# Kernel optimization log

Measured on AMD Instinct MI355X. Metric: run time of the kernel, lower is better.

Reference implementation:

```python
import jax, jax.numpy as jnp
import numpy as np

D = 1024
H = 4
HD = D // H
WIN = 128
NPMEM = 4
EPS = 1e-5


def _layernorm(x, g, b):
    mu = jnp.mean(x, axis=-1, keepdims=True)
    var = jnp.var(x, axis=-1, keepdims=True)
    return (x - mu) * jax.lax.rsqrt(var + EPS) * g + b


def _rotate_half(t):
    h = t.shape[-1] // 2
    return jnp.concatenate([-t[..., h:], t[..., :h]], axis=-1)


def setup_inputs() -> dict:
    key = jax.random.key(0)
    ks = jax.random.split(key, 20)
    B, L = 2, 4096
    s = 0.02
    inp = {
        'x': jax.random.normal(ks[0], (B, L, D), jnp.float32),
        'cos': jax.random.uniform(ks[1], (L + 8, HD), jnp.float32),
        'sin': jax.random.uniform(ks[2], (L + 8, HD), jnp.float32),
        'global_out': jax.random.normal(ks[3], (B, L, D), jnp.float32),
        'local_out': jax.random.normal(ks[4], (B, L, D), jnp.float32),
        'wq': jax.random.normal(ks[5], (D, D), jnp.float32) * s,
        'wk': jax.random.normal(ks[6], (D, D), jnp.float32) * s,
        'wv': jax.random.normal(ks[7], (D, D), jnp.float32) * s,
        'wo_attn': jax.random.normal(ks[8], (D, D), jnp.float32) * s,
        'pmem': jax.random.normal(ks[9], (1, NPMEM, D), jnp.float32),
        'gate_w': jax.random.normal(ks[10], (3 * D, 3 * D), jnp.float32) * s,
        'gate_b': jnp.zeros((3 * D,), jnp.float32),
        'outproj_w': jax.random.normal(ks[11], (3 * D, D), jnp.float32) * s,
        'outproj_b': jnp.zeros((D,), jnp.float32),
        'ln_mem_g': jnp.ones((D,), jnp.float32),
        'ln_mem_b': jnp.zeros((D,), jnp.float32),
        'ln_mlp_g': jnp.ones((D,), jnp.float32),
        'ln_mlp_b': jnp.zeros((D,), jnp.float32),
        'fc1_w': jax.random.normal(ks[12], (D, 4 * D), jnp.float32) * s,
        'fc1_b': jnp.zeros((4 * D,), jnp.float32),
        'fc2_w': jax.random.normal(ks[13], (4 * D, D), jnp.float32) * s,
        'fc2_b': jnp.zeros((D,), jnp.float32),
    }
    return inp


def reference(x, cos, sin, global_out, local_out, wq, wk, wv, wo_attn, pmem,
              gate_w, gate_b, outproj_w, outproj_b, ln_mem_g, ln_mem_b,
              ln_mlp_g, ln_mlp_b, fc1_w, fc1_b, fc2_w, fc2_b):
    B, L, _ = x.shape
    residual = x

    # prepend persistent memory tokens
    xp = jnp.concatenate([jnp.broadcast_to(pmem, (B, NPMEM, D)), x], axis=1)
    Lt = L + NPMEM

    q = (xp @ wq).reshape(B, Lt, H, HD)
    k = (xp @ wk).reshape(B, Lt, H, HD)
    v = (xp @ wv).reshape(B, Lt, H, HD)

    # rotary embedding over the full pmem+seq length
    cc = cos[:Lt][None, :, None, :]
    ss = sin[:Lt][None, :, None, :]
    q = q * cc + _rotate_half(q) * ss
    k = k * cc + _rotate_half(k) * ss

    i = jnp.arange(Lt)[:, None]
    j = jnp.arange(Lt)[None, :]
    mask = (j <= i) & (j >= i - WIN)  # [Lt, Lt]

    scale = 1.0 / jnp.sqrt(jnp.asarray(HD, x.dtype))
    scores = jnp.einsum('blhd,bmhd->bhlm', q, k) * scale
    scores = jnp.where(mask[None, None], scores, jnp.finfo(scores.dtype).min)
    attn = jax.nn.softmax(scores, axis=-1)
    out = jnp.einsum('bhlm,bmhd->blhd', attn, v).reshape(B, Lt, D)
    core_out = (out @ wo_attn)[:, -L:, :]

    combined = jnp.concatenate([global_out, local_out, core_out], axis=-1)
    g = jax.nn.sigmoid(combined @ gate_w + gate_b)
    memory_output = (combined * g) @ outproj_w + outproj_b

    x1 = residual + _layernorm(memory_output, ln_mem_g, ln_mem_b)
    xn = _layernorm(x1, ln_mlp_g, ln_mlp_b)
    mlp_out = jax.nn.silu(xn @ fc1_w + fc1_b) @ fc2_w + fc2_b
    return x1 + mlp_out
```

## Files before the change

kernel.cpp:

```cpp
#include <hip/hip_runtime.h>
#include <stdint.h>

#define D_    1024
#define H_    4
#define HD_   256
#define WIN_  128
#define NPM_  4
#define B_    2
#define L_    4096
#define LT_   4100
#define LTP_  4112
#define QKL_  2048

typedef __attribute__((ext_vector_type(8))) short short8;
typedef __attribute__((ext_vector_type(4))) float f32x4;

__device__ __forceinline__ short f2bf(float f) {
  union { float f; uint32_t u; } v; v.f = f;
  uint32_t r = v.u + 0x7FFFu + ((v.u >> 16) & 1u);
  return (short)(r >> 16);
}
__device__ __forceinline__ float bf2f(short h) {
  union { uint32_t u; float f; } v; v.u = ((uint32_t)(uint16_t)h) << 16;
  return v.f;
}

typedef __attribute__((address_space(1))) void GAS;
typedef __attribute__((address_space(3))) void LAS;
__device__ __forceinline__ void gl16(const void* g, void* l) {
  __builtin_amdgcn_global_load_lds((GAS*)g, (LAS*)l, 16, 0, 0);
}
__device__ __forceinline__ void waitvm0() { asm volatile("s_waitcnt vmcnt(0)" ::: "memory"); }

#define EP_BF16 0
#define EP_F32B 1
#define EP_GATE 2
#define EP_SILU 3
#define EP_RES  4
#define EP_CORE 5
#define EP_VT   6

template<int EP, int TM>
__global__ __launch_bounds__(256, 4)
void gemm_bt(const short* __restrict__ A, int lda,
             const short* __restrict__ Bt,
             void* __restrict__ Cp, int ldc,
             const float* __restrict__ bias,
             const void* __restrict__ aux, int ldaux,
             int M, int N, int K)
{
  constexpr int WM = TM / 2;
  constexpr int MT = WM / 16;
  constexpr int BUFSZ = (TM + 128) * 32;
  __shared__ __attribute__((aligned(16))) short lds[2 * BUFSZ];
  const int tid  = threadIdx.x;
  const int lane = tid & 63, wave = tid >> 6;
  const int lhi  = lane >> 4, llo = lane & 15;
  const int m0 = blockIdx.x * TM, n0 = blockIdx.y * 128;
  const int mw = (wave >> 1) * WM, nw = (wave & 1) * 64;

  const int srow = tid >> 2;
  const int sg   = (tid & 3) ^ ((tid >> 3) & 3);
  const short* pA0 = A + (size_t)min(m0 + srow, M - 1) * lda + sg * 8;
  const short* pA1 = (TM == 128) ? A + (size_t)min(m0 + srow + 64, M - 1) * lda + sg * 8 : pA0;
  const short* pB0 = Bt + (size_t)(n0 + srow) * K + sg * 8;
  const short* pB1 = Bt + (size_t)(n0 + srow + 64) * K + sg * 8;

  const int segoff = (lhi ^ ((llo >> 1) & 3)) * 8;

  auto stage = [&](int b, int i) {
    const int k = i << 5;
    short* base = &lds[b * BUFSZ];
    gl16(pA0 + k, &base[tid * 8]);
    if constexpr (TM == 128) gl16(pA1 + k, &base[2048 + tid * 8]);
    gl16(pB0 + k, &base[TM * 32 + tid * 8]);
    gl16(pB1 + k, &base[TM * 32 + 2048 + tid * 8]);
  };

  f32x4 acc[MT][4];
#pragma unroll
  for (int i = 0; i < MT; i++)
#pragma unroll
    for (int j = 0; j < 4; j++) acc[i][j] = f32x4{0.f, 0.f, 0.f, 0.f};

  const int NI = K >> 5;
  stage(0, 0);
  waitvm0();
  __syncthreads();

  for (int i = 0; i < NI; i++) {
    if (i + 1 < NI) stage((i + 1) & 1, i + 1);
    const short* bufp = &lds[(i & 1) * BUFSZ];
    short8 af[MT], bfr[4];
#pragma unroll
    for (int mt = 0; mt < MT; mt++)
      af[mt] = *(const short8*)&bufp[(mw + mt * 16 + llo) * 32 + segoff];
#pragma unroll
    for (int nt = 0; nt < 4; nt++)
      bfr[nt] = *(const short8*)&bufp[TM * 32 + (nw + nt * 16 + llo) * 32 + segoff];
#pragma unroll
    for (int mt = 0; mt < MT; mt++)
#pragma unroll
      for (int nt = 0; nt < 4; nt++)
        acc[mt][nt] = __builtin_amdgcn_mfma_f32_16x16x32_bf16(af[mt], bfr[nt], acc[mt][nt], 0, 0, 0);
    waitvm0();
    __syncthreads();
  }

  const int gcb = n0 + nw;
#pragma unroll
  for (int mt = 0; mt < MT; mt++) {
    const int gr0 = m0 + mw + mt * 16 + lhi * 4;
#pragma unroll
    for (int nt = 0; nt < 4; nt++) {
      const int gc = gcb + nt * 16 + llo;
      float bv = 0.f;
      if constexpr (EP != EP_BF16 && EP != EP_CORE && EP != EP_VT) bv = bias[gc];
#pragma unroll
      for (int r = 0; r < 4; r++) {
        const int gr = gr0 + r;
        if (gr >= M) continue;
        const float v = acc[mt][nt][r];
        if constexpr (EP == EP_VT) {
          if (gc < N) {
            const int b   = gc >= LT_ ? 1 : 0;
            const int tok = gc - b * LT_;
            const int hh  = gr >> 8, dd = gr & 255;
            ((short*)Cp)[(size_t)((b * H_ + hh) * HD_ + dd) * ldc + tok] = f2bf(v);
          }
          continue;
        }
        if constexpr (EP == EP_CORE) {
          const int b   = gr >= LT_ ? 1 : 0;
          const int tok = gr - b * LT_;
          if (tok >= NPM_) {
            const int cr = b * L_ + (tok - NPM_);
            ((short*)Cp)[(size_t)cr * ldc + gc] = f2bf(v);
          }
          continue;
        }
        const size_t idx = (size_t)gr * ldc + gc;
        if constexpr (EP == EP_BF16) {
          ((short*)Cp)[idx] = f2bf(v);
        } else if constexpr (EP == EP_F32B) {
          ((float*)Cp)[idx] = v + bv;
        } else if constexpr (EP == EP_GATE) {
          float g  = 1.f / (1.f + __expf(-(v + bv)));
          float cv = bf2f(((const short*)aux)[(size_t)gr * ldaux + gc]);
          ((short*)Cp)[idx] = f2bf(cv * g);
        } else if constexpr (EP == EP_SILU) {
          float xx = v + bv;
          ((short*)Cp)[idx] = f2bf(xx / (1.f + __expf(-xx)));
        } else {
          ((float*)Cp)[idx] = v + bv + ((const float*)aux)[(size_t)gr * ldaux + gc];
        }
      }
    }
  }
}

struct TAll {
  const float* src[8];
  short* dst[8];
  int C[8];
  int R[8];
  int nbx[8];
  int start[8];
};

__global__ __launch_bounds__(256)
void transpose_all(TAll t)
{
  __shared__ short tile[32][33];
  const int bid = blockIdx.x;
  int w = 0;
#pragma unroll
  for (int i = 1; i < 8; i++) w = (bid >= t.start[i]) ? i : w;
  const int rel = bid - t.start[w];
  const int nbx = t.nbx[w];
  const int bx = rel % nbx, by = rel / nbx;
  const float* src = t.src[w];
  short* dst = t.dst[w];
  const int ld_in = t.C[w], ld_out = t.R[w];
  const int r0 = by * 32, c0 = bx * 32;
  const int tx = threadIdx.x & 31, ty = threadIdx.x >> 5;
#pragma unroll
  for (int i = 0; i < 4; i++)
    tile[ty + i * 8][tx] = f2bf(src[(size_t)(r0 + ty + i * 8) * ld_in + c0 + tx]);
  __syncthreads();
#pragma unroll
  for (int i = 0; i < 4; i++)
    dst[(size_t)(c0 + ty + i * 8) * ld_out + r0 + tx] = tile[tx][ty + i * 8];
}

__global__ __launch_bounds__(256)
void prep_k(const float* __restrict__ x, const float* __restrict__ pmem,
            const float* __restrict__ go, const float* __restrict__ lo,
            short* __restrict__ xp, short* __restrict__ comb)
{
  const int bid = blockIdx.x;
  if (bid < 8200) {
    int gid = bid * 256 + threadIdx.x;
    int row = gid >> 8;
    int c4  = (gid & 255) * 4;
    int b   = row >= LT_ ? 1 : 0;
    int tok = row - b * LT_;
    const float* src = (tok < NPM_) ? (pmem + (size_t)tok * D_ + c4)
                                    : (x + ((size_t)b * L_ + tok - NPM_) * D_ + c4);
    float4 v = *(const float4*)src;
    short o[4] = {f2bf(v.x), f2bf(v.y), f2bf(v.z), f2bf(v.w)};
    *(short4*)&xp[(size_t)row * D_ + c4] = *(short4*)o;
  } else {
    int gid = (bid - 8200) * 256 + threadIdx.x;
    int row = gid >> 9;
    int c4  = (gid & 511) * 4;
    const float* src = (c4 < D_) ? (go + (size_t)row * D_ + c4)
                                 : (lo + (size_t)row * D_ + (c4 - D_));
    float4 v = *(const float4*)src;
    short o[4] = {f2bf(v.x), f2bf(v.y), f2bf(v.z), f2bf(v.w)};
    *(short4*)&comb[(size_t)row * 3072 + c4] = *(short4*)o;
  }
}

__global__ __launch_bounds__(256)
void rope_kernel(short* __restrict__ qkv,
                 const float* __restrict__ cosp, const float* __restrict__ sinp)
{
  int gid = blockIdx.x * 256 + threadIdx.x;
  int d   = (gid & 31) * 4;
  int h   = (gid >> 5) & 3;
  int row = gid >> 7;
  int t   = row >= LT_ ? row - LT_ : row;
  size_t base = (size_t)row * QKL_ + h * HD_ + d;
  float4 cl = *(const float4*)&cosp[(size_t)t * HD_ + d];
  float4 ch = *(const float4*)&cosp[(size_t)t * HD_ + d + 128];
  float4 sl = *(const float4*)&sinp[(size_t)t * HD_ + d];
  float4 sh = *(const float4*)&sinp[(size_t)t * HD_ + d + 128];
  short4 ql4 = *(const short4*)&qkv[base],        qh4 = *(const short4*)&qkv[base + 128];
  short4 kl4 = *(const short4*)&qkv[base + 1024], kh4 = *(const short4*)&qkv[base + 1152];
  const float SC = 1.f / 16.f;
  short oql[4], oqh[4], okl[4], okh[4];
#pragma unroll
  for (int j = 0; j < 4; j++) {
    float c0 = ((float*)&cl)[j], c1 = ((float*)&ch)[j];
    float s0 = ((float*)&sl)[j], s1 = ((float*)&sh)[j];
    float ql = bf2f(((short*)&ql4)[j]), qh = bf2f(((short*)&qh4)[j]);
    float kl = bf2f(((short*)&kl4)[j]), kh = bf2f(((short*)&kh4)[j]);
    oql[j] = f2bf((ql * c0 - qh * s0) * SC);
    oqh[j] = f2bf((qh * c1 + ql * s1) * SC);
    okl[j] = f2bf(kl * c0 - kh * s0);
    okh[j] = f2bf(kh * c1 + kl * s1);
  }
  *(short4*)&qkv[base]        = *(short4*)oql;
  *(short4*)&qkv[base + 128]  = *(short4*)oqh;
  *(short4*)&qkv[base + 1024] = *(short4*)okl;
  *(short4*)&qkv[base + 1152] = *(short4*)okh;
}

__global__ __launch_bounds__(256, 2)
void attn_kernel(const short* __restrict__ qkv, const short* __restrict__ vT,
                 short* __restrict__ outp)
{
  __shared__ short lKV[256 * 72];
  __shared__ short lP[64 * 200];
  const int tid  = threadIdx.x;
  const int lane = tid & 63, wave = tid >> 6;
  const int lhi  = lane >> 4, llo = lane & 15;
  const int i0 = blockIdx.x * 64;
  const int h = blockIdx.y, b = blockIdx.z;
  const int kw0 = i0 - 128;
  const size_t vbase = (size_t)(b * H_ + h) * HD_ * LTP_;

  short8 qf[8];
  {
    int ic = min(i0 + wave * 16 + llo, LT_ - 1);
    const short* qrow = qkv + (size_t)(b * LT_ + ic) * QKL_ + h * HD_;
#pragma unroll
    for (int ks = 0; ks < 8; ks++)
      qf[ks] = *(const short8*)(qrow + ks * 32 + lhi * 8);
  }

  f32x4 S[12];
#pragma unroll
  for (int st = 0; st < 12; st++) S[st] = f32x4{0.f, 0.f, 0.f, 0.f};

  for (int kc = 0; kc < 3; kc++) {
    if (kc) __syncthreads();
    {
      int row = tid >> 2;
      int jc = min(max(kw0 + kc * 64 + row, 0), LT_ - 1);
      const short* krow = qkv + (size_t)(b * LT_ + jc) * QKL_ + 1024 + h * HD_;
#pragma unroll
      for (int it = 0; it < 8; it++) {
        int seg = (tid & 3) + it * 4;
        *(short8*)&lKV[row * 264 + seg * 8] = *(const short8*)(krow + seg * 8);
      }
    }
    __syncthreads();
#pragma unroll
    for (int ks = 0; ks < 8; ks++) {
#pragma unroll
      for (int nt = 0; nt < 4; nt++) {
        short8 bf = *(const short8*)&lKV[(nt * 16 + llo) * 264 + ks * 32 + lhi * 8];
        S[kc * 4 + nt] = __builtin_amdgcn_mfma_f32_16x16x32_bf16(qf[ks], bf, S[kc * 4 + nt], 0, 0, 0);
      }
    }
  }

  const int irow = i0 + wave * 16 + lhi * 4;
  float mx[4], sm[4];
#pragma unroll
  for (int r = 0; r < 4; r++) mx[r] = -3.0e38f;
#pragma unroll
  for (int st = 0; st < 12; st++) {
    int j = kw0 + st * 16 + llo;
#pragma unroll
    for (int r = 0; r < 4; r++) {
      int i = irow + r;
      bool ok = (j >= 0) & (j <= i) & (j >= i - WIN_);
      float s = ok ? S[st][r] : -1.0e30f;
      S[st][r] = s;
      mx[r] = fmaxf(mx[r], s);
    }
  }
#pragma unroll
  for (int r = 0; r < 4; r++)
#pragma unroll
    for (int o = 1; o < 16; o <<= 1) mx[r] = fmaxf(mx[r], __shfl_xor(mx[r], o));
#pragma unroll
  for (int r = 0; r < 4; r++) sm[r] = 0.f;
#pragma unroll
  for (int st = 0; st < 12; st++)
#pragma unroll
    for (int r = 0; r < 4; r++) {
      float e = __expf(S[st][r] - mx[r]);
      S[st][r] = e;
      sm[r] += e;
    }
#pragma unroll
  for (int r = 0; r < 4; r++) {
#pragma unroll
    for (int o = 1; o < 16; o <<= 1) sm[r] += __shfl_xor(sm[r], o);
    sm[r] = 1.f / sm[r];
  }

#pragma unroll
  for (int st = 0; st < 12; st++)
#pragma unroll
    for (int r = 0; r < 4; r++)
      lP[(wave * 16 + lhi * 4 + r) * 200 + st * 16 + llo] = f2bf(S[st][r] * sm[r]);

  f32x4 O[16];
#pragma unroll
  for (int nt = 0; nt < 16; nt++) O[nt] = f32x4{0.f, 0.f, 0.f, 0.f};

  for (int kc = 0; kc < 3; kc++) {
    __syncthreads();
#pragma unroll
    for (int it = 0; it < 8; it++) {
      int id = it * 256 + tid;
      int d = id >> 3, seg = id & 7;
      int kbase = min(max(kw0 + kc * 64 + seg * 8, 0), LTP_ - 8);
      *(short8*)&lKV[d * 72 + seg * 8] = *(const short8*)&vT[vbase + (size_t)d * LTP_ + kbase];
    }
    __syncthreads();
#pragma unroll
    for (int ks = 0; ks < 2; ks++) {
      short8 pf = *(const short8*)&lP[(wave * 16 + llo) * 200 + kc * 64 + ks * 32 + lhi * 8];
#pragma unroll
      for (int nt = 0; nt < 16; nt++) {
        short8 vf = *(const short8*)&lKV[(nt * 16 + llo) * 72 + ks * 32 + lhi * 8];
        O[nt] = __builtin_amdgcn_mfma_f32_16x16x32_bf16(pf, vf, O[nt], 0, 0, 0);
      }
    }
  }

  short* orow = outp + (size_t)(b * LT_) * D_ + h * HD_;
#pragma unroll
  for (int nt = 0; nt < 16; nt++)
#pragma unroll
    for (int r = 0; r < 4; r++) {
      int i = irow + r;
      if (i < LT_) orow[(size_t)i * D_ + nt * 16 + llo] = f2bf(O[nt][r]);
    }
}

__global__ __launch_bounds__(256, 4)
void ln2_kernel(const float* __restrict__ mo, const float* __restrict__ xres,
                const float* __restrict__ g1, const float* __restrict__ b1,
                const float* __restrict__ g2, const float* __restrict__ b2,
                float* __restrict__ x1, short* __restrict__ xn)
{
  const int row = blockIdx.x;
  const int tid = threadIdx.x;
  const int lane = tid & 63, wave = tid >> 6;
  __shared__ float red[8], red2[8];
  float4 v = ((const float4*)(mo + (size_t)row * D_))[tid];
  float s = v.x + v.y + v.z + v.w;
  float s2 = v.x * v.x + v.y * v.y + v.z * v.z + v.w * v.w;
#pragma unroll
  for (int o = 1; o < 64; o <<= 1) { s += __shfl_xor(s, o); s2 += __shfl_xor(s2, o); }
  if (lane == 0) { red[wave] = s; red[wave + 4] = s2; }
  __syncthreads();
  float S = red[0] + red[1] + red[2] + red[3];
  float S2 = red[4] + red[5] + red[6] + red[7];
  float mu = S * (1.f / D_);
  float rs = rsqrtf(S2 * (1.f / D_) - mu * mu + 1e-5f);
  float4 gg = ((const float4*)g1)[tid];
  float4 bb = ((const float4*)b1)[tid];
  float4 xv = ((const float4*)(xres + (size_t)row * D_))[tid];
  float4 o1;
  o1.x = xv.x + (v.x - mu) * rs * gg.x + bb.x;
  o1.y = xv.y + (v.y - mu) * rs * gg.y + bb.y;
  o1.z = xv.z + (v.z - mu) * rs * gg.z + bb.z;
  o1.w = xv.w + (v.w - mu) * rs * gg.w + bb.w;
  ((float4*)(x1 + (size_t)row * D_))[tid] = o1;
  s = o1.x + o1.y + o1.z + o1.w;
  s2 = o1.x * o1.x + o1.y * o1.y + o1.z * o1.z + o1.w * o1.w;
#pragma unroll
  for (int o = 1; o < 64; o <<= 1) { s += __shfl_xor(s, o); s2 += __shfl_xor(s2, o); }
  if (lane == 0) { red2[wave] = s; red2[wave + 4] = s2; }
  __syncthreads();
  S = red2[0] + red2[1] + red2[2] + red2[3];
  S2 = red2[4] + red2[5] + red2[6] + red2[7];
  float mu2 = S * (1.f / D_);
  float rs2 = rsqrtf(S2 * (1.f / D_) - mu2 * mu2 + 1e-5f);
  float4 g2v = ((const float4*)g2)[tid];
  float4 b2v = ((const float4*)b2)[tid];
  short o2[4];
  o2[0] = f2bf((o1.x - mu2) * rs2 * g2v.x + b2v.x);
  o2[1] = f2bf((o1.y - mu2) * rs2 * g2v.y + b2v.y);
  o2[2] = f2bf((o1.z - mu2) * rs2 * g2v.z + b2v.z);
  o2[3] = f2bf((o1.w - mu2) * rs2 * g2v.w + b2v.w);
  *(short4*)&xn[(size_t)row * D_ + tid * 4] = *(short4*)o2;
}

extern "C" void kernel_launch(void* const* d_in, const int* in_sizes, int n_in,
                              void* d_out, int out_size, void* d_ws, size_t ws_size,
                              hipStream_t stream)
{
  const float* x      = (const float*)d_in[0];
  const float* cosp   = (const float*)d_in[1];
  const float* sinp   = (const float*)d_in[2];
  const float* go     = (const float*)d_in[3];
  const float* lo     = (const float*)d_in[4];
  const float* wq     = (const float*)d_in[5];
  const float* wk     = (const float*)d_in[6];
  const float* wv     = (const float*)d_in[7];
  const float* wo     = (const float*)d_in[8];
  const float* pmem   = (const float*)d_in[9];
  const float* gate_w = (const float*)d_in[10];
  const float* gate_b = (const float*)d_in[11];
  const float* outp_w = (const float*)d_in[12];
  const float* outp_b = (const float*)d_in[13];
  const float* ln1g   = (const float*)d_in[14];
  const float* ln1b   = (const float*)d_in[15];
  const float* ln2g   = (const float*)d_in[16];
  const float* ln2b   = (const float*)d_in[17];
  const float* fc1w   = (const float*)d_in[18];
  const float* fc1b   = (const float*)d_in[19];
  const float* fc2w   = (const float*)d_in[20];
  const float* fc2b   = (const float*)d_in[21];
  float* out = (float*)d_out;
  char* p = (char*)d_ws;

  short* wqkvT = (short*)(p + 0);
  short* woT   = (short*)(p + 6291456);
  short* gateT = (short*)(p + 8388608);
  short* outpT = (short*)(p + 27262976);
  short* fc1T  = (short*)(p + 33554432);
  short* fc2T  = (short*)(p + 41943040);
  short* comb  = (short*)(p + 50331648);
  char*  pool  = p + 100663296;
  short* xp    = (short*)(pool);
  short* qkv   = (short*)(pool + 16793600);
  short* vT    = (short*)(pool + 67174400);
  short* a_o   = (short*)(pool + 84017152);
  short* gated = (short*)(pool);
  short* h1    = (short*)(pool);
  float* mo    = (float*)(pool + 67174400);
  float* x1    = (float*)(comb);
  short* xn    = (short*)((char*)comb + 33554432);

  TAll t;
  const float* srcs[8] = {wq, wk, wv, wo, gate_w, outp_w, fc1w, fc2w};
  short* dsts[8] = {wqkvT, wqkvT + 1048576, wqkvT + 2097152, woT, gateT, outpT, fc1T, fc2T};
  const int Rs[8] = {1024, 1024, 1024, 1024, 3072, 3072, 1024, 4096};
  const int Cs[8] = {1024, 1024, 1024, 1024, 3072, 1024, 4096, 1024};
  int cum = 0;
  for (int i = 0; i < 8; i++) {
    t.src[i] = srcs[i]; t.dst[i] = dsts[i];
    t.R[i] = Rs[i]; t.C[i] = Cs[i]; t.nbx[i] = Cs[i] / 32;
    t.start[i] = cum;
    cum += (Cs[i] / 32) * (Rs[i] / 32);
  }
  transpose_all<<<cum, 256, 0, stream>>>(t);

  prep_k<<<24584, 256, 0, stream>>>(x, pmem, go, lo, xp, comb);

  const int Mq = B_ * LT_;
  gemm_bt<EP_BF16, 128><<<dim3(65, 16), 256, 0, stream>>>(xp, 1024, wqkvT, qkv, QKL_, nullptr, nullptr, 0, Mq, 2048, 1024);
  gemm_bt<EP_VT, 128><<<dim3(8, 65), 256, 0, stream>>>(wqkvT + 2097152, 1024, xp, vT, LTP_, nullptr, nullptr, 0, 1024, 8200, 1024);

  rope_kernel<<<4100, 256, 0, stream>>>(qkv, cosp, sinp);

  attn_kernel<<<dim3(65, H_, B_), 256, 0, stream>>>(qkv, vT, a_o);

  gemm_bt<EP_CORE, 128><<<dim3(65, 8), 256, 0, stream>>>(
      a_o, 1024, woT, comb + 2048, 3072, nullptr, nullptr, 0, Mq, 1024, 1024);

  gemm_bt<EP_GATE, 128><<<dim3(64, 24), 256, 0, stream>>>(comb, 3072, gateT, gated, 3072, gate_b, comb, 3072, 8192, 3072, 3072);

  gemm_bt<EP_F32B, 128><<<dim3(64, 8), 256, 0, stream>>>(gated, 3072, outpT, mo, 1024, outp_b, nullptr, 0, 8192, 1024, 3072);

  ln2_kernel<<<8192, 256, 0, stream>>>(mo, x, ln1g, ln1b, ln2g, ln2b, x1, xn);

  gemm_bt<EP_SILU, 128><<<dim3(64, 32), 256, 0, stream>>>(xn, 1024, fc1T, h1, 4096, fc1b, nullptr, 0, 8192, 4096, 1024);
  gemm_bt<EP_RES, 128><<<dim3(64, 8), 256, 0, stream>>>(h1, 4096, fc2T, out, 1024, fc2b, x1, 1024, 8192, 1024, 4096);
}
```

Measured before the change: 921.4 us.

## Fuse RoPE into attention, merge QKV/VT GEMMs and init kernels into single launches

Removes the standalone rope kernel and applies rotary embedding to Q fragments in registers and to K tiles while staging them into LDS inside the attention kernel. The QK and V-transposed GEMMs become one launch, and the weight transpose and input prep kernels become one launch. This saves the rope pass's read and write of Q/K and cuts launch count. In exchange K rotation is recomputed for each overlapping window tile, which adds cos/sin loads and ALU work to the attention kernel.

```diff
diff --git a/kernel.cpp b/kernel.cpp
--- a/kernel.cpp
+++ b/kernel.cpp
@@ -41,22 +41,21 @@
 #define EP_VT   6
 
 template<int EP, int TM>
-__global__ __launch_bounds__(256, 4)
-void gemm_bt(const short* __restrict__ A, int lda,
-             const short* __restrict__ Bt,
-             void* __restrict__ Cp, int ldc,
-             const float* __restrict__ bias,
-             const void* __restrict__ aux, int ldaux,
-             int M, int N, int K)
+__device__ __forceinline__ void gemm_body(
+    short* lds, int m0, int n0,
+    const short* __restrict__ A, int lda,
+    const short* __restrict__ Bt,
+    void* __restrict__ Cp, int ldc,
+    const float* __restrict__ bias,
+    const void* __restrict__ aux, int ldaux,
+    int M, int N, int K)
 {
   constexpr int WM = TM / 2;
   constexpr int MT = WM / 16;
   constexpr int BUFSZ = (TM + 128) * 32;
-  __shared__ __attribute__((aligned(16))) short lds[2 * BUFSZ];
   const int tid  = threadIdx.x;
   const int lane = tid & 63, wave = tid >> 6;
   const int lhi  = lane >> 4, llo = lane & 15;
-  const int m0 = blockIdx.x * TM, n0 = blockIdx.y * 128;
   const int mw = (wave >> 1) * WM, nw = (wave & 1) * 64;
 
   const int srow = tid >> 2;
@@ -159,6 +158,41 @@
   }
 }
 
+template<int EP, int TM>
+__global__ __launch_bounds__(256, 4)
+void gemm_bt(const short* __restrict__ A, int lda,
+             const short* __restrict__ Bt,
+             void* __restrict__ Cp, int ldc,
+             const float* __restrict__ bias,
+             const void* __restrict__ aux, int ldaux,
+             int M, int N, int K)
+{
+  __shared__ __attribute__((aligned(16))) short lds[2 * (TM + 128) * 32];
+  gemm_body<EP, TM>(lds, blockIdx.x * TM, blockIdx.y * 128,
+                    A, lda, Bt, Cp, ldc, bias, aux, ldaux, M, N, K);
+}
+
+__global__ __launch_bounds__(256, 4)
+void gemm_qkvt(const short* __restrict__ xp, const short* __restrict__ wqkT,
+               short* __restrict__ qkv,
+               const short* __restrict__ wvT, short* __restrict__ vT)
+{
+  __shared__ __attribute__((aligned(16))) short lds[2 * 256 * 32];
+  const int bid = blockIdx.x;
+  if (bid < 1040) {
+    const int bx = bid % 65, by = bid / 65;
+    gemm_body<EP_BF16, 128>(lds, bx * 128, by * 128,
+                            xp, 1024, wqkT, qkv, QKL_, nullptr, nullptr, 0,
+                            B_ * LT_, 2048, 1024);
+  } else {
+    const int b2 = bid - 1040;
+    const int bx = b2 % 8, by = b2 / 8;
+    gemm_body<EP_VT, 128>(lds, bx * 128, by * 128,
+                          wvT, 1024, xp, vT, LTP_, nullptr, nullptr, 0,
+                          1024, B_ * LT_, 1024);
+  }
+}
+
 struct TAll {
   const float* src[8];
   short* dst[8];
@@ -169,51 +203,45 @@
 };
 
 __global__ __launch_bounds__(256)
-void transpose_all(TAll t)
+void init_k(TAll t, const float* __restrict__ x, const float* __restrict__ pmem,
+            const float* __restrict__ go, const float* __restrict__ lo,
+            short* __restrict__ xp, short* __restrict__ comb)
 {
   __shared__ short tile[32][33];
   const int bid = blockIdx.x;
-  int w = 0;
-#pragma unroll
-  for (int i = 1; i < 8; i++) w = (bid >= t.start[i]) ? i : w;
-  const int rel = bid - t.start[w];
-  const int nbx = t.nbx[w];
-  const int bx = rel % nbx, by = rel / nbx;
-  const float* src = t.src[w];
-  short* dst = t.dst[w];
-  const int ld_in = t.C[w], ld_out = t.R[w];
-  const int r0 = by * 32, c0 = bx * 32;
-  const int tx = threadIdx.x & 31, ty = threadIdx.x >> 5;
-#pragma unroll
-  for (int i = 0; i < 4; i++)
-    tile[ty + i * 8][tx] = f2bf(src[(size_t)(r0 + ty + i * 8) * ld_in + c0 + tx]);
-  __syncthreads();
-#pragma unroll
-  for (int i = 0; i < 4; i++)
-    dst[(size_t)(c0 + ty + i * 8) * ld_out + r0 + tx] = tile[tx][ty + i * 8];
-}
-
-__global__ __launch_bounds__(256)
-void prep_k(const float* __restrict__ x, const float* __restrict__ pmem,
-            const float* __restrict__ go, const float* __restrict__ lo,
-            short* __restrict__ xp, short* __restrict__ comb)
-{
-  const int bid = blockIdx.x;
-  if (bid < 8200) {
-    int gid = bid * 256 + threadIdx.x;
-    int row = gid >> 8;
-    int c4  = (gid & 255) * 4;
-    int b   = row >= LT_ ? 1 : 0;
-    int tok = row - b * LT_;
+  if (bid < 24576) {
+    int w = 0;
+#pragma unroll
+    for (int i = 1; i < 8; i++) w = (bid >= t.start[i]) ? i : w;
+    const int rel = bid - t.start[w];
+    const int nbx = t.nbx[w];
+    const int bx = rel % nbx, by = rel / nbx;
+    const float* src = t.src[w];
+    short* dst = t.dst[w];
+    const int ld_in = t.C[w], ld_out = t.R[w];
+    const int r0 = by * 32, c0 = bx * 32;
+    const int tx = threadIdx.x & 31, ty = threadIdx.x >> 5;
+#pragma unroll
+    for (int i = 0; i < 4; i++)
+      tile[ty + i * 8][tx] = f2bf(src[(size_t)(r0 + ty + i * 8) * ld_in + c0 + tx]);
+    __syncthreads();
+#pragma unroll
+    for (int i = 0; i < 4; i++)
+      dst[(size_t)(c0 + ty + i * 8) * ld_out + r0 + tx] = tile[tx][ty + i * 8];
+  } else if (bid < 24576 + 8200) {
+    const int row = bid - 24576;
+    const int c4  = threadIdx.x * 4;
+    const int b   = row >= LT_ ? 1 : 0;
+    const int tok = row - b * LT_;
     const float* src = (tok < NPM_) ? (pmem + (size_t)tok * D_ + c4)
                                     : (x + ((size_t)b * L_ + tok - NPM_) * D_ + c4);
     float4 v = *(const float4*)src;
     short o[4] = {f2bf(v.x), f2bf(v.y), f2bf(v.z), f2bf(v.w)};
     *(short4*)&xp[(size_t)row * D_ + c4] = *(short4*)o;
   } else {
-    int gid = (bid - 8200) * 256 + threadIdx.x;
-    int row = gid >> 9;
-    int c4  = (gid & 511) * 4;
+    const int gid = (bid - 24576 - 8200) * 256 + threadIdx.x;
+    const int row = gid >> 9;
+    const int c4  = (gid & 511) * 4;
     const float* src = (c4 < D_) ? (go + (size_t)row * D_ + c4)
                                  : (lo + (size_t)row * D_ + (c4 - D_));
     float4 v = *(const float4*)src;
@@ -222,43 +250,9 @@
   }
 }
 
-__global__ __launch_bounds__(256)
-void rope_kernel(short* __restrict__ qkv,
-                 const float* __restrict__ cosp, const float* __restrict__ sinp)
-{
-  int gid = blockIdx.x * 256 + threadIdx.x;
-  int d   = (gid & 31) * 4;
-  int h   = (gid >> 5) & 3;
-  int row = gid >> 7;
-  int t   = row >= LT_ ? row - LT_ : row;
-  size_t base = (size_t)row * QKL_ + h * HD_ + d;
-  float4 cl = *(const float4*)&cosp[(size_t)t * HD_ + d];
-  float4 ch = *(const float4*)&cosp[(size_t)t * HD_ + d + 128];
-  float4 sl = *(const float4*)&sinp[(size_t)t * HD_ + d];
-  float4 sh = *(const float4*)&sinp[(size_t)t * HD_ + d + 128];
-  short4 ql4 = *(const short4*)&qkv[base],        qh4 = *(const short4*)&qkv[base + 128];
-  short4 kl4 = *(const short4*)&qkv[base + 1024], kh4 = *(const short4*)&qkv[base + 1152];
-  const float SC = 1.f / 16.f;
-  short oql[4], oqh[4], okl[4], okh[4];
-#pragma unroll
-  for (int j = 0; j < 4; j++) {
-    float c0 = ((float*)&cl)[j], c1 = ((float*)&ch)[j];
-    float s0 = ((float*)&sl)[j], s1 = ((float*)&sh)[j];
-    float ql = bf2f(((short*)&ql4)[j]), qh = bf2f(((short*)&qh4)[j]);
-    float kl = bf2f(((short*)&kl4)[j]), kh = bf2f(((short*)&kh4)[j]);
-    oql[j] = f2bf((ql * c0 - qh * s0) * SC);
-    oqh[j] = f2bf((qh * c1 + ql * s1) * SC);
-    okl[j] = f2bf(kl * c0 - kh * s0);
-    okh[j] = f2bf(kh * c1 + kl * s1);
-  }
-  *(short4*)&qkv[base]        = *(short4*)oql;
-  *(short4*)&qkv[base + 128]  = *(short4*)oqh;
-  *(short4*)&qkv[base + 1024] = *(short4*)okl;
-  *(short4*)&qkv[base + 1152] = *(short4*)okh;
-}
-
 __global__ __launch_bounds__(256, 2)
 void attn_kernel(const short* __restrict__ qkv, const short* __restrict__ vT,
+                 const float* __restrict__ cosp, const float* __restrict__ sinp,
                  short* __restrict__ outp)
 {
   __shared__ short lKV[256 * 72];
@@ -273,11 +267,36 @@
 
   short8 qf[8];
   {
-    int ic = min(i0 + wave * 16 + llo, LT_ - 1);
+    const int ic = min(i0 + wave * 16 + llo, LT_ - 1);
     const short* qrow = qkv + (size_t)(b * LT_ + ic) * QKL_ + h * HD_;
+    const float* cr = cosp + (size_t)ic * HD_;
+    const float* sr = sinp + (size_t)ic * HD_;
 #pragma unroll
     for (int ks = 0; ks < 8; ks++)
       qf[ks] = *(const short8*)(qrow + ks * 32 + lhi * 8);
+    const float SC = 1.f / 16.f;
+#pragma unroll
+    for (int ks = 0; ks < 4; ks++) {
+      const int d0 = ks * 32 + lhi * 8;
+      float cl[8], ch[8], sl[8], sh[8];
+      *(float4*)&cl[0] = *(const float4*)&cr[d0];
+      *(float4*)&cl[4] = *(const float4*)&cr[d0 + 4];
+      *(float4*)&ch[0] = *(const float4*)&cr[d0 + 128];
+      *(float4*)&ch[4] = *(const float4*)&cr[d0 + 132];
+      *(float4*)&sl[0] = *(const float4*)&sr[d0];
+      *(float4*)&sl[4] = *(const float4*)&sr[d0 + 4];
+      *(float4*)&sh[0] = *(const float4*)&sr[d0 + 128];
+      *(float4*)&sh[4] = *(const float4*)&sr[d0 + 132];
+      short lo8[8], hi8[8];
+#pragma unroll
+      for (int j = 0; j < 8; j++) {
+        float ql = bf2f(qf[ks][j]), qh = bf2f(qf[ks + 4][j]);
+        lo8[j] = f2bf((ql * cl[j] - qh * sl[j]) * SC);
+        hi8[j] = f2bf((qh * ch[j] + ql * sh[j]) * SC);
+      }
+      qf[ks]     = *(short8*)lo8;
+      qf[ks + 4] = *(short8*)hi8;
+    }
   }
 
   f32x4 S[12];
@@ -287,13 +306,39 @@
   for (int kc = 0; kc < 3; kc++) {
     if (kc) __syncthreads();
     {
-      int row = tid >> 2;
-      int jc = min(max(kw0 + kc * 64 + row, 0), LT_ - 1);
+      const int row = tid >> 2;
+      const int jc = min(max(kw0 + kc * 64 + row, 0), LT_ - 1);
       const short* krow = qkv + (size_t)(b * LT_ + jc) * QKL_ + 1024 + h * HD_;
+      const float* cr = cosp + (size_t)jc * HD_;
+      const float* sr = sinp + (size_t)jc * HD_;
+      short8 kv[8];
 #pragma unroll
       for (int it = 0; it < 8; it++) {
-        int seg = (tid & 3) + it * 4;
-        *(short8*)&lKV[row * 264 + seg * 8] = *(const short8*)(krow + seg * 8);
+        const int seg = (tid & 3) + it * 4;
+        kv[it] = *(const short8*)(krow + seg * 8);
+      }
+#pragma unroll
+      for (int it = 0; it < 4; it++) {
+        const int segl = (tid & 3) + it * 4;
+        const int d0 = segl * 8;
+        float cl[8], ch[8], sl[8], sh[8];
+        *(float4*)&cl[0] = *(const float4*)&cr[d0];
+        *(float4*)&cl[4] = *(const float4*)&cr[d0 + 4];
+        *(float4*)&ch[0] = *(const float4*)&cr[d0 + 128];
+        *(float4*)&ch[4] = *(const float4*)&cr[d0 + 132];
+        *(float4*)&sl[0] = *(const float4*)&sr[d0];
+        *(float4*)&sl[4] = *(const float4*)&sr[d0 + 4];
+        *(float4*)&sh[0] = *(const float4*)&sr[d0 + 128];
+        *(float4*)&sh[4] = *(const float4*)&sr[d0 + 132];
+        short lo8[8], hi8[8];
+#pragma unroll
+        for (int j = 0; j < 8; j++) {
+          float kl = bf2f(kv[it][j]), kh = bf2f(kv[it + 4][j]);
+          lo8[j] = f2bf(kl * cl[j] - kh * sl[j]);
+          hi8[j] = f2bf(kh * ch[j] + kl * sh[j]);
+        }
+        *(short8*)&lKV[row * 264 + segl * 8]        = *(short8*)lo8;
+        *(short8*)&lKV[row * 264 + (segl + 16) * 8] = *(short8*)hi8;
       }
     }
     __syncthreads();
@@ -494,18 +539,13 @@
     t.start[i] = cum;
     cum += (Cs[i] / 32) * (Rs[i] / 32);
   }
-  transpose_all<<<cum, 256, 0, stream>>>(t);
-
-  prep_k<<<24584, 256, 0, stream>>>(x, pmem, go, lo, xp, comb);
+  init_k<<<24576 + 8200 + 16384, 256, 0, stream>>>(t, x, pmem, go, lo, xp, comb);
+
+  gemm_qkvt<<<1560, 256, 0, stream>>>(xp, wqkvT, qkv, wqkvT + 2097152, vT);
+
+  attn_kernel<<<dim3(65, H_, B_), 256, 0, stream>>>(qkv, vT, cosp, sinp, a_o);
 
   const int Mq = B_ * LT_;
-  gemm_bt<EP_BF16, 128><<<dim3(65, 16), 256, 0, stream>>>(xp, 1024, wqkvT, qkv, QKL_, nullptr, nullptr, 0, Mq, 2048, 1024);
-  gemm_bt<EP_VT, 128><<<dim3(8, 65), 256, 0, stream>>>(wqkvT + 2097152, 1024, xp, vT, LTP_, nullptr, nullptr, 0, 1024, 8200, 1024);
-
-  rope_kernel<<<4100, 256, 0, stream>>>(qkv, cosp, sinp);
-
-  attn_kernel<<<dim3(65, H_, B_), 256, 0, stream>>>(qkv, vT, a_o);
-
   gemm_bt<EP_CORE, 128><<<dim3(65, 8), 256, 0, stream>>>(
       a_o, 1024, woT, comb + 2048, 3072, nullptr, nullptr, 0, Mq, 1024, 1024);
 
```

After: 935.7 us. No clear change (+1.6%).
